# Optimization experiments

Hardware: AMD Instinct MI355X
Metric: run time of the kernel (lower is better)

Reference implementation:

```python
import jax, jax.numpy as jnp
import numpy as np

N = 50000
E = 1600000
IN_DIM = 64
EMB_DIM = 64
DENSE = 128
HEADS = 2
GATD = 64
SLOPE = 0.2


def gat_conv(x, src, dst, W, al, ar, b):
    # DGL GATConv: x [N, Fin], W [Fin, H*D], al/ar/b [H, D]
    n = x.shape[0]
    H, D = al.shape
    z = (x @ W).reshape(n, H, D)                      # [N,H,D]
    el = jnp.sum(z * al, axis=-1)                     # [N,H]
    er = jnp.sum(z * ar, axis=-1)                     # [N,H]
    e = jax.nn.leaky_relu(el[src] + er[dst], SLOPE)   # [E,H]
    # edge softmax grouped by destination node
    m = jax.ops.segment_max(e, dst, num_segments=n)   # [N,H]
    ex = jnp.exp(e - m[dst])                          # [E,H]
    s = jax.ops.segment_sum(ex, dst, num_segments=n)  # [N,H]
    alpha = ex / s[dst]                               # [E,H]
    out = jax.ops.segment_sum(alpha[:, :, None] * z[src], dst, num_segments=n)
    return out + b                                    # [N,H,D]


def setup_inputs() -> dict:
    key = jax.random.key(0)
    ks = jax.random.split(key, 20)
    g = lambda k, sh: jax.random.normal(k, sh, dtype=jnp.float32) * 0.05
    inp = {
        "feat": jax.random.normal(ks[0], (N, IN_DIM), dtype=jnp.float32),
        "node_ids": jax.random.randint(ks[1], (N,), 0, N, dtype=jnp.int32),
        "src": jax.random.randint(ks[2], (E,), 0, N, dtype=jnp.int32),
        "dst": jax.random.randint(ks[3], (E,), 0, N, dtype=jnp.int32),
        "emb": g(ks[4], (N, EMB_DIM)),
        "dense_w": g(ks[5], (IN_DIM + EMB_DIM, DENSE)),
        "dense_b": jnp.zeros((DENSE,), jnp.float32),
        "g1_w": g(ks[6], (DENSE, HEADS * GATD)),
        "g1_al": g(ks[7], (HEADS, GATD)),
        "g1_ar": g(ks[8], (HEADS, GATD)),
        "g1_b": jnp.zeros((HEADS, GATD), jnp.float32),
        "g2_w": g(ks[9], (HEADS * GATD, HEADS * GATD)),
        "g2_al": g(ks[10], (HEADS, GATD)),
        "g2_ar": g(ks[11], (HEADS, GATD)),
        "g2_b": jnp.zeros((HEADS, GATD), jnp.float32),
        "out_w": g(ks[12], (HEADS * GATD, 1)),
        "out_al": g(ks[13], (1, 1)),
        "out_ar": g(ks[14], (1, 1)),
        "out_b": jnp.zeros((1, 1), jnp.float32),
    }
    return inp


def reference(feat, node_ids, src, dst, emb, dense_w, dense_b,
              g1_w, g1_al, g1_ar, g1_b, g2_w, g2_al, g2_ar, g2_b,
              out_w, out_al, out_ar, out_b):
    # embedding concat + initial dense + ReLU
    h = jnp.concatenate([emb[node_ids], feat], axis=-1)   # [N, 128]
    h = jax.nn.relu(h @ dense_w + dense_b)                # [N, 128]
    # GAT layer 1: ReLU then concat heads (reshape N, H*D)
    h = jax.nn.relu(gat_conv(h, src, dst, g1_w, g1_al, g1_ar, g1_b))
    h = h.reshape(h.shape[0], -1)                         # [N, H*D]
    # GAT layer 2
    h = jax.nn.relu(gat_conv(h, src, dst, g2_w, g2_al, g2_ar, g2_b))
    h = h.reshape(h.shape[0], -1)
    # output GAT layer, 1 head, squeeze head dim
    h = gat_conv(h, src, dst, out_w, out_al, out_ar, out_b)  # [N,1,1]
    return h[:, 0, :]                                        # [N,1]
```

## Files before the change

kernel.cpp:

```cpp
#include <hip/hip_runtime.h>
#include <cfloat>
#include <cmath>


#define CBG 256
#define CAPC 12288
#define TILE 2048
#define BIMG 10240

typedef __attribute__((ext_vector_type(8))) short short8v;
typedef __attribute__((ext_vector_type(4))) float f32x4;

__device__ __forceinline__ float lrelu(float x) { return x > 0.f ? x : 0.2f * x; }

__device__ __forceinline__ uint32_t bf16_rne(float f) {
  uint32_t u = __float_as_uint(f);
  return (u + 0x7fffu + ((u >> 16) & 1u)) >> 16;
}
__device__ __forceinline__ uint32_t pack_hilo(float v) {
  uint32_t h = bf16_rne(v);
  float r = v - __uint_as_float(h << 16);
  return (h << 16) | bf16_rne(r);
}

__global__ __launch_bounds__(256) void prep_kernel(
    const float* __restrict__ W0, const float* __restrict__ W1,
    const float* __restrict__ W2, short* __restrict__ Whi0,
    short* __restrict__ Wlo0, short* __restrict__ Whi1, short* __restrict__ Wlo1,
    short* __restrict__ Whi2, short* __restrict__ Wlo2,
    int* __restrict__ scount, int ncb) {
  if (blockIdx.x >= 24) {
    for (int i = threadIdx.x; i < ncb; i += 256) scount[i] = 0;
    return;
  }
  int which = blockIdx.x >> 3;
  const float* W = which == 0 ? W0 : (which == 1 ? W1 : W2);
  short* Whi = which == 0 ? Whi0 : (which == 1 ? Whi1 : Whi2);
  short* Wlo = which == 0 ? Wlo0 : (which == 1 ? Wlo1 : Wlo2);
  int fid = (blockIdx.x & 7) * 256 + threadIdx.x;
  int lane = fid & 63;
  int cq = fid >> 6;
  int q = cq >> 3, c = cq & 7;
  int col = c * 16 + (lane & 15);
  int k0 = q * 32 + (lane >> 4) * 8;
#pragma unroll
  for (int j = 0; j < 8; j++) {
    float v = W[(k0 + j) * 128 + col];
    uint32_t h = bf16_rne(v);
    float r = v - __uint_as_float(h << 16);
    Whi[fid * 8 + j] = (short)h;
    Wlo[fid * 8 + j] = (short)bf16_rne(r);
  }
}

__global__ __launch_bounds__(256) void bucketA_kernel(
    const int* __restrict__ src, const int* __restrict__ dst,
    int* __restrict__ scount, uint32_t* __restrict__ tmp, int e, int ncb) {
  __shared__ int cnt[256];
  __shared__ int lscan[256];
  __shared__ int gbase[256];
  __shared__ uint32_t image[TILE];
  const int t = threadIdx.x;
  const int e0 = blockIdx.x * TILE;
  const int ne = min(TILE, e - e0);

  for (int i = t; i < 256; i += 256) cnt[i] = 0;
  __syncthreads();
  for (int i = t; i < ne; i += 256) atomicAdd(&cnt[dst[e0 + i] >> 8], 1);
  __syncthreads();
  if (t < 64) {
    int carry = 0;
    for (int base = 0; base < ncb; base += 64) {
      int idx = base + t;
      int c = (idx < ncb) ? cnt[idx] : 0;
      int v = c;
#pragma unroll
      for (int off = 1; off < 64; off <<= 1) {
        int u = __shfl_up(v, off, 64);
        if (t >= off) v += u;
      }
      if (idx < ncb) lscan[idx] = carry + v - c;
      carry += __shfl(v, 63, 64);
    }
  }
  __syncthreads();
  for (int b = t; b < ncb; b += 256)
    gbase[b] = (cnt[b] > 0) ? atomicAdd(&scount[b], cnt[b]) : 0;
  __syncthreads();
  for (int b = t; b < ncb; b += 256) cnt[b] = 0;
  __syncthreads();
  for (int i = t; i < ne; i += 256) {
    int d = dst[e0 + i], s = src[e0 + i];
    int b = d >> 8;
    int r = atomicAdd(&cnt[b], 1);
    image[lscan[b] + r] =
        (uint32_t)s | ((uint32_t)(d & 255) << 16) | ((uint32_t)b << 24);
  }
  __syncthreads();
  for (int j = t; j < ne; j += 256) {
    uint32_t w = image[j];
    int b = w >> 24;
    int pos = gbase[b] + (j - lscan[b]);
    if (pos < CAPC) tmp[(size_t)b * CAPC + pos] = w & 0xFFFFFFu;
  }
}

__device__ __forceinline__ void bucketB_body(
    int b, char* smem, const uint32_t* __restrict__ tmp,
    const int* __restrict__ scount, int* __restrict__ row_start,
    int* __restrict__ csr_src, int n, int ncb, int e) {
  int* cnt = (int*)smem;
  int* cur = cnt + 256;
  int* wsum = cur + 256;
  int* s_base = wsum + 4;
  uint32_t* image = (uint32_t*)(smem + 2080);
  const int t = threadIdx.x, lane = t & 63, wid = t >> 6;

  if (t < 64) {
    int part = 0;
    for (int idx = lane; idx < b; idx += 64) part += scount[idx];
#pragma unroll
    for (int off = 32; off; off >>= 1) part += __shfl_xor(part, off, 64);
    if (lane == 0) *s_base = part;
  }
  cnt[t] = 0;
  __syncthreads();
  const int total = min(scount[b], CAPC);
  const int base = *s_base;
  const uint32_t* strm = tmp + (size_t)b * CAPC;

  for (int i = t; i < total; i += 256) atomicAdd(&cnt[(strm[i] >> 16) & 255], 1);
  __syncthreads();
  int c = cnt[t], v = c;
#pragma unroll
  for (int off = 1; off < 64; off <<= 1) {
    int u = __shfl_up(v, off, 64);
    if (lane >= off) v += u;
  }
  if (lane == 63) wsum[wid] = v;
  __syncthreads();
  if (t == 0) {
    int acc = 0;
#pragma unroll
    for (int w = 0; w < 4; w++) { int x = wsum[w]; wsum[w] = acc; acc += x; }
  }
  __syncthreads();
  int ex = wsum[wid] + v - c;
  cur[t] = ex;
  int d = b * CBG + t;
  if (d < n) row_start[d] = base + ex;
  if (b == 0 && t == 0) row_start[n] = e;
  __syncthreads();
  for (int i = t; i < total; i += 256) {
    uint32_t w = strm[i];
    int dl = (w >> 16) & 255;
    int pos = atomicAdd(&cur[dl], 1);
    if (pos < BIMG) image[pos] = w & 0xFFFFu;
    else csr_src[base + pos] = (int)(w & 0xFFFFu);
  }
  __syncthreads();
  const int lim = total < BIMG ? total : BIMG;
  for (int j = t; j < lim; j += 256) csr_src[base + j] = (int)image[j];
}

template <int MODE>
__device__ __forceinline__ void mfmm_body(
    int bid, char* smem,
    const uint32_t* __restrict__ Xp, const short* __restrict__ Whi,
    const short* __restrict__ Wlo, const float* __restrict__ bias,
    uint32_t* __restrict__ Hp, uint32_t* __restrict__ zp,
    float2* __restrict__ el2, float2* __restrict__ er2,
    const float* __restrict__ al, const float* __restrict__ ar, int n,
    const float* __restrict__ emb, const int* __restrict__ ids,
    const float* __restrict__ feat) {
  short* Ahi = (short*)smem;
  short* Alo = Ahi + 64 * 136;
  const int t = threadIdx.x;
  const int nb = bid * 64;

  for (int idx = t; idx < 64 * 32; idx += 256) {
    int nl = idx >> 5, k4 = (idx & 31) << 2;
    int node = nb + nl;
    uint32_t h01 = 0, h23 = 0, l01 = 0, l23 = 0;
    if (node < n) {
      if (MODE == 1) {
        uint4 w = *(const uint4*)&Xp[(size_t)node * 128 + k4];
        h01 = (w.x >> 16) | (w.y & 0xffff0000u);
        l01 = (w.x & 0xffffu) | (w.y << 16);
        h23 = (w.z >> 16) | (w.w & 0xffff0000u);
        l23 = (w.z & 0xffffu) | (w.w << 16);
      } else {
        float4 v;
        if (k4 < 64) v = *(const float4*)&emb[(size_t)ids[node] * 64 + k4];
        else         v = *(const float4*)&feat[(size_t)node * 64 + (k4 - 64)];
        uint32_t a0 = bf16_rne(v.x), a1 = bf16_rne(v.y);
        uint32_t a2 = bf16_rne(v.z), a3 = bf16_rne(v.w);
        h01 = a0 | (a1 << 16);
        h23 = a2 | (a3 << 16);
        l01 = bf16_rne(v.x - __uint_as_float(a0 << 16)) |
              (bf16_rne(v.y - __uint_as_float(a1 << 16)) << 16);
        l23 = bf16_rne(v.z - __uint_as_float(a2 << 16)) |
              (bf16_rne(v.w - __uint_as_float(a3 << 16)) << 16);
      }
    }
    *(uint2*)&Ahi[nl * 136 + k4] = make_uint2(h01, h23);
    *(uint2*)&Alo[nl * 136 + k4] = make_uint2(l01, l23);
  }
  __syncthreads();

  const int lane = t & 63, wv = t >> 6;
  const int r16 = lane & 15, g = lane >> 4;
  const int arow = (wv * 16 + r16) * 136;

  f32x4 acc[8];
#pragma unroll
  for (int c = 0; c < 8; c++) acc[c] = (f32x4){0.f, 0.f, 0.f, 0.f};

#pragma unroll
  for (int q = 0; q < 4; q++) {
    int ka = q * 32 + g * 8;
    short8v ahi = *(const short8v*)&Ahi[arow + ka];
    short8v alo = *(const short8v*)&Alo[arow + ka];
#pragma unroll
    for (int c = 0; c < 8; c++) {
      short8v bhi = *(const short8v*)&Whi[(((q * 8 + c) * 64) + lane) * 8];
      short8v blo = *(const short8v*)&Wlo[(((q * 8 + c) * 64) + lane) * 8];
      acc[c] = __builtin_amdgcn_mfma_f32_16x16x32_bf16(ahi, bhi, acc[c], 0, 0, 0);
      acc[c] = __builtin_amdgcn_mfma_f32_16x16x32_bf16(ahi, blo, acc[c], 0, 0, 0);
      acc[c] = __builtin_amdgcn_mfma_f32_16x16x32_bf16(alo, bhi, acc[c], 0, 0, 0);
    }
  }

  const int node_base = nb + wv * 16;
  if (MODE == 0) {
#pragma unroll
    for (int c = 0; c < 8; c++) {
      int col = c * 16 + r16;
      float bv = bias[col];
#pragma unroll
      for (int r = 0; r < 4; r++) {
        int node = node_base + g * 4 + r;
        if (node < n) {
          float v = fmaxf(acc[c][r] + bv, 0.f);
          Hp[(size_t)node * 128 + col] = pack_hilo(v);
        }
      }
    }
  } else {
    float p0l[4] = {0, 0, 0, 0}, p1l[4] = {0, 0, 0, 0};
    float p0r[4] = {0, 0, 0, 0}, p1r[4] = {0, 0, 0, 0};
#pragma unroll
    for (int c = 0; c < 8; c++) {
      int col = c * 16 + r16;
      float av = al[col], rv = ar[col];
#pragma unroll
      for (int r = 0; r < 4; r++) {
        if (c < 4) { p0l[r] = fmaf(acc[c][r], av, p0l[r]); p0r[r] = fmaf(acc[c][r], rv, p0r[r]); }
        else       { p1l[r] = fmaf(acc[c][r], av, p1l[r]); p1r[r] = fmaf(acc[c][r], rv, p1r[r]); }
      }
    }
#pragma unroll
    for (int c = 0; c < 8; c++) {
#pragma unroll
      for (int r = 0; r < 4; r++) {
        float other = __shfl_xor(acc[c][r], 1, 64);
        int node = node_base + g * 4 + r;
        if (!(lane & 1) && node < n) {
          uint32_t w = bf16_rne(acc[c][r]) | (bf16_rne(other) << 16);
          zp[(size_t)node * 64 + c * 8 + (r16 >> 1)] = w;
        }
      }
    }
#pragma unroll
    for (int off = 1; off < 16; off <<= 1) {
#pragma unroll
      for (int r = 0; r < 4; r++) {
        p0l[r] += __shfl_xor(p0l[r], off, 64);
        p1l[r] += __shfl_xor(p1l[r], off, 64);
        p0r[r] += __shfl_xor(p0r[r], off, 64);
        p1r[r] += __shfl_xor(p1r[r], off, 64);
      }
    }
    if (r16 == 0) {
#pragma unroll
      for (int r = 0; r < 4; r++) {
        int node = node_base + g * 4 + r;
        if (node < n) {
          el2[node] = make_float2(p0l[r], p1l[r]);
          er2[node] = make_float2(p0r[r], p1r[r]);
        }
      }
    }
  }
}

__global__ __launch_bounds__(256) void mfmm0_bktB_kernel(
    const uint32_t* __restrict__ tmp, const int* __restrict__ scount,
    int* __restrict__ row_start, int* __restrict__ csr_src, int ncbB,
    const short* __restrict__ Whi, const short* __restrict__ Wlo,
    const float* __restrict__ bias, uint32_t* __restrict__ Hp, int n, int ncb,
    int e, const float* __restrict__ emb, const int* __restrict__ ids,
    const float* __restrict__ feat) {
  __shared__ __align__(16) char smem[43040];
  if ((int)blockIdx.x < ncbB) {
    bucketB_body(blockIdx.x, smem, tmp, scount, row_start, csr_src, n, ncb, e);
  } else {
    mfmm_body<0>(blockIdx.x - ncbB, smem, nullptr, Whi, Wlo, bias, Hp,
                 nullptr, nullptr, nullptr, nullptr, nullptr, n, emb, ids, feat);
  }
}

__global__ __launch_bounds__(256) void mfmm1_kernel(
    const uint32_t* __restrict__ Xp, const short* __restrict__ Whi,
    const short* __restrict__ Wlo, uint32_t* __restrict__ zp,
    float2* __restrict__ el2, float2* __restrict__ er2,
    const float* __restrict__ al, const float* __restrict__ ar, int n) {
  __shared__ __align__(16) char smem[64 * 136 * 2 * 2];
  mfmm_body<1>(blockIdx.x, smem, Xp, Whi, Wlo, nullptr, nullptr, zp, el2, er2,
               al, ar, n, nullptr, nullptr, nullptr);
}

__global__ void hist_kernel(const int* __restrict__ dst, int* __restrict__ cnt, int e) {
  for (int i = blockIdx.x * blockDim.x + threadIdx.x; i < e; i += gridDim.x * blockDim.x)
    atomicAdd(&cnt[dst[i]], 1);
}
__global__ void scatter_kernel(const int* __restrict__ src, const int* __restrict__ dst,
                               const int* __restrict__ row_start, int* __restrict__ cursor,
                               int* __restrict__ csr_src, int e) {
  for (int i = blockIdx.x * blockDim.x + threadIdx.x; i < e; i += gridDim.x * blockDim.x) {
    int d = dst[i];
    int pos = atomicAdd(&cursor[d], 1);
    csr_src[row_start[d] + pos] = src[i];
  }
}
__global__ __launch_bounds__(1024) void scan1_kernel(const int* __restrict__ cnt,
                                                     int* __restrict__ row_start,
                                                     int* __restrict__ bsum, int n) {
  __shared__ int wsum[16];
  const int t = threadIdx.x, lane = t & 63, wid = t >> 6;
  int i = blockIdx.x * 1024 + t;
  int c = (i < n) ? cnt[i] : 0;
  int v = c;
#pragma unroll
  for (int off = 1; off < 64; off <<= 1) {
    int u = __shfl_up(v, off, 64);
    if (lane >= off) v += u;
  }
  if (lane == 63) wsum[wid] = v;
  __syncthreads();
  if (t == 0) {
    int acc = 0;
#pragma unroll
    for (int w = 0; w < 16; w++) { int x = wsum[w]; wsum[w] = acc; acc += x; }
    bsum[blockIdx.x] = acc;
  }
  __syncthreads();
  if (i < n) row_start[i] = wsum[wid] + v - c;
}
__global__ __launch_bounds__(64) void scan2_kernel(int* __restrict__ bsum, int nb) {
  const int lane = threadIdx.x;
  int carry = 0;
  for (int base = 0; base < nb; base += 64) {
    int idx = base + lane;
    int c = (idx < nb) ? bsum[idx] : 0;
    int v = c;
#pragma unroll
    for (int off = 1; off < 64; off <<= 1) {
      int u = __shfl_up(v, off, 64);
      if (lane >= off) v += u;
    }
    if (idx < nb) bsum[idx] = carry + v - c;
    carry += __shfl(v, 63, 64);
  }
}
__global__ void scan3_kernel(int* __restrict__ row_start, const int* __restrict__ bsum,
                             int n, int e) {
  int i = blockIdx.x * blockDim.x + threadIdx.x;
  if (i < n) row_start[i] += bsum[i >> 10];
  if (i == 0) row_start[n] = e;
}

#define CAP 256
__global__ __launch_bounds__(256) void agg12_kernel(
    const uint32_t* __restrict__ zp, const float2* __restrict__ el2,
    const float2* __restrict__ er2, const int* __restrict__ row_start,
    const int* __restrict__ csr_src, const float* __restrict__ bias,
    uint32_t* __restrict__ Hp,
    const float* __restrict__ ow, const float* __restrict__ oal,
    const float* __restrict__ oar, float* __restrict__ z3,
    float* __restrict__ el3, float* __restrict__ er3, int n, int fuse_out) {
  __shared__ float2 ec[4][CAP];
  __shared__ int sc[4][CAP];
  const int w = threadIdx.x >> 6, lane = threadIdx.x & 63;
  const int node = blockIdx.x * 4 + w;
  const bool valid = node < n;
  int rs = 0, deg = 0;
  float er0 = 0.f, er1 = 0.f;
  if (valid) {
    rs = row_start[node];
    deg = row_start[node + 1] - rs;
    float2 e2 = er2[node];
    er0 = e2.x; er1 = e2.y;
  }
  const int cdeg = deg < CAP ? deg : CAP;

  float sp0 = 0.f, sp1 = 0.f;
  for (int i = lane; i < deg; i += 64) {
    int s = csr_src[rs + i];
    float2 l = el2[s];
    float x0 = __expf(lrelu(l.x + er0));
    float x1 = __expf(lrelu(l.y + er1));
    if (i < CAP) { sc[w][i] = s; ec[w][i] = make_float2(x0, x1); }
    sp0 += x0; sp1 += x1;
  }
#pragma unroll
  for (int off = 32; off; off >>= 1) {
    sp0 += __shfl_xor(sp0, off, 64);
    sp1 += __shfl_xor(sp1, off, 64);
  }
  __syncthreads();

  float ae = 0.f, ao = 0.f;
  int i = 0;
  for (; i + 8 <= cdeg; i += 8) {
    uint32_t zw[8];
    float xh[8];
#pragma unroll
    for (int u = 0; u < 8; u++) {
      int s = sc[w][i + u];
      float2 ex = ec[w][i + u];
      xh[u] = (lane < 32) ? ex.x : ex.y;
      zw[u] = zp[(size_t)s * 64 + lane];
    }
#pragma unroll
    for (int u = 0; u < 8; u++) {
      ae = fmaf(xh[u], __uint_as_float(zw[u] << 16), ae);
      ao = fmaf(xh[u], __uint_as_float(zw[u] & 0xffff0000u), ao);
    }
  }
  for (; i < cdeg; i++) {
    int s = sc[w][i];
    float2 ex = ec[w][i];
    float x = (lane < 32) ? ex.x : ex.y;
    uint32_t zw = zp[(size_t)s * 64 + lane];
    ae = fmaf(x, __uint_as_float(zw << 16), ae);
    ao = fmaf(x, __uint_as_float(zw & 0xffff0000u), ao);
  }
  for (; i < deg; i++) {
    int s = csr_src[rs + i];
    float2 l = el2[s];
    float x0 = __expf(lrelu(l.x + er0));
    float x1 = __expf(lrelu(l.y + er1));
    float x = (lane < 32) ? x0 : x1;
    uint32_t zw = zp[(size_t)s * 64 + lane];
    ae = fmaf(x, __uint_as_float(zw << 16), ae);
    ao = fmaf(x, __uint_as_float(zw & 0xffff0000u), ao);
  }

  if (valid) {
    float sp = (lane < 32) ? sp0 : sp1;
    float2 b2 = reinterpret_cast<const float2*>(bias)[lane];
    float oe, oo;
    if (deg == 0) { oe = b2.x; oo = b2.y; }
    else { oe = ae / sp + b2.x; oo = ao / sp + b2.y; }
    oe = fmaxf(oe, 0.f);
    oo = fmaxf(oo, 0.f);
    if (!fuse_out) {
      *(uint2*)&Hp[(size_t)node * 128 + 2 * lane] =
          make_uint2(pack_hilo(oe), pack_hilo(oo));
    } else {
      float2 w2 = reinterpret_cast<const float2*>(ow)[lane];
      float d = oe * w2.x + oo * w2.y;
#pragma unroll
      for (int off = 32; off; off >>= 1) d += __shfl_xor(d, off, 64);
      if (lane == 0) {
        z3[node] = d;
        el3[node] = d * oal[0];
        er3[node] = d * oar[0];
      }
    }
  }
}

__global__ __launch_bounds__(256) void agg3_kernel(
    const float* __restrict__ z3, const float* __restrict__ el3,
    const float* __restrict__ er3, const int* __restrict__ row_start,
    const int* __restrict__ csr_src, const float* __restrict__ b,
    float* __restrict__ out, int n) {
  int node = blockIdx.x * 8 + (threadIdx.x >> 5);
  int l32 = threadIdx.x & 31;
  if (node >= n) return;
  int rs = row_start[node];
  int deg = row_start[node + 1] - rs;
  float er = er3[node];
  float sp = 0.f, ap = 0.f;
  for (int i = l32; i < deg; i += 32) {
    int s = csr_src[rs + i];
    float ex = __expf(lrelu(el3[s] + er));
    sp += ex;
    ap = fmaf(ex, z3[s], ap);
  }
#pragma unroll
  for (int off = 16; off; off >>= 1) {
    sp += __shfl_xor(sp, off, 64);
    ap += __shfl_xor(ap, off, 64);
  }
  if (l32 == 0) out[node] = (deg == 0) ? b[0] : (ap / sp + b[0]);
}

extern "C" void kernel_launch(void* const* d_in, const int* in_sizes, int n_in,
                              void* d_out, int out_size, void* d_ws, size_t ws_size,
                              hipStream_t stream) {
  const float* feat     = (const float*)d_in[0];
  const int*   node_ids = (const int*)d_in[1];
  const int*   src      = (const int*)d_in[2];
  const int*   dst      = (const int*)d_in[3];
  const float* emb      = (const float*)d_in[4];
  const float* dense_w  = (const float*)d_in[5];
  const float* dense_b  = (const float*)d_in[6];
  const float* g1_w     = (const float*)d_in[7];
  const float* g1_al    = (const float*)d_in[8];
  const float* g1_ar    = (const float*)d_in[9];
  const float* g1_b     = (const float*)d_in[10];
  const float* g2_w     = (const float*)d_in[11];
  const float* g2_al    = (const float*)d_in[12];
  const float* g2_ar    = (const float*)d_in[13];
  const float* g2_b     = (const float*)d_in[14];
  const float* out_w    = (const float*)d_in[15];
  const float* out_al   = (const float*)d_in[16];
  const float* out_ar   = (const float*)d_in[17];
  const float* out_b    = (const float*)d_in[18];
  const int n = in_sizes[0] / 64;
  const int e = in_sizes[2];

  const int ncb = (n + CBG - 1) / CBG;

  char* ws = (char*)d_ws;
  size_t off = 0;
  auto alloc = [&](size_t bytes) -> void* {
    void* p = ws + off;
    off += (bytes + 255) & ~(size_t)255;
    return p;
  };
  uint32_t* Hp       = (uint32_t*)alloc((size_t)n * 128 * 4);
  size_t zp_bytes    = (size_t)n * 64 * 4;
  size_t tmp_bytes   = (size_t)ncb * CAPC * 4;
  uint32_t* zp       = (uint32_t*)alloc(zp_bytes > tmp_bytes ? zp_bytes : tmp_bytes);
  uint32_t* tmp      = zp;
  float2*   el2      = (float2*)alloc((size_t)n * 8);
  float2*   er2      = (float2*)alloc((size_t)n * 8);
  float*    z3       = (float*)alloc((size_t)n * 4);
  float*    el3      = (float*)alloc((size_t)n * 4);
  float*    er3      = (float*)alloc((size_t)n * 4);
  int*      scount   = (int*)alloc((size_t)ncb * 4);
  int*      row_start= (int*)alloc((size_t)(n + 1) * 4);
  int*      csr_src  = (int*)alloc((size_t)e * 4);
  short*    Wd_hi    = (short*)alloc(2048 * 8 * 2);
  short*    Wd_lo    = (short*)alloc(2048 * 8 * 2);
  short*    W1_hi    = (short*)alloc(2048 * 8 * 2);
  short*    W1_lo    = (short*)alloc(2048 * 8 * 2);
  short*    W2_hi    = (short*)alloc(2048 * 8 * 2);
  short*    W2_lo    = (short*)alloc(2048 * 8 * 2);
  int*      cnt      = (int*)alloc((size_t)n * 4);
  int*      cursor   = (int*)alloc((size_t)n * 4);
  const int nblk     = (n + 1023) / 1024;
  int*      bsum     = (int*)alloc((size_t)nblk * 4);

  const int mmgrid = (n + 63) / 64;
  const int ngrid4 = (n + 3) / 4;
  const int ngrid8 = (n + 7) / 8;

  prep_kernel<<<25, 256, 0, stream>>>(dense_w, g1_w, g2_w,
                                      Wd_hi, Wd_lo, W1_hi, W1_lo, W2_hi, W2_lo,
                                      scount, ncb);

  if (n < 65536) {
    const int natile = (e + TILE - 1) / TILE;
    bucketA_kernel<<<natile, 256, 0, stream>>>(src, dst, scount, tmp, e, ncb);
    mfmm0_bktB_kernel<<<ncb + mmgrid, 256, 0, stream>>>(
        tmp, scount, row_start, csr_src, ncb,
        Wd_hi, Wd_lo, dense_b, Hp, n, ncb, e, emb, node_ids, feat);
  } else {
    hipMemsetAsync(cnt, 0, (size_t)n * 4, stream);
    hipMemsetAsync(cursor, 0, (size_t)n * 4, stream);
    hist_kernel<<<2048, 256, 0, stream>>>(dst, cnt, e);
    scan1_kernel<<<nblk, 1024, 0, stream>>>(cnt, row_start, bsum, n);
    scan2_kernel<<<1, 64, 0, stream>>>(bsum, nblk);
    scan3_kernel<<<(n + 255) / 256, 256, 0, stream>>>(row_start, bsum, n, e);
    scatter_kernel<<<2048, 256, 0, stream>>>(src, dst, row_start, cursor, csr_src, e);
    mfmm0_bktB_kernel<<<mmgrid, 256, 0, stream>>>(
        tmp, scount, row_start, csr_src, 0,
        Wd_hi, Wd_lo, dense_b, Hp, n, ncb, e, emb, node_ids, feat);
  }

  mfmm1_kernel<<<mmgrid, 256, 0, stream>>>(Hp, W1_hi, W1_lo, zp, el2, er2,
                                           g1_al, g1_ar, n);
  agg12_kernel<<<ngrid4, 256, 0, stream>>>(zp, el2, er2, row_start, csr_src, g1_b, Hp,
                                           nullptr, nullptr, nullptr, nullptr, nullptr,
                                           nullptr, n, 0);
  mfmm1_kernel<<<mmgrid, 256, 0, stream>>>(Hp, W2_hi, W2_lo, zp, el2, er2,
                                           g2_al, g2_ar, n);
  agg12_kernel<<<ngrid4, 256, 0, stream>>>(zp, el2, er2, row_start, csr_src, g2_b, nullptr,
                                           out_w, out_al, out_ar, z3, el3, er3, n, 1);
  agg3_kernel<<<ngrid8, 256, 0, stream>>>(z3, el3, er3, row_start, csr_src, out_b,
                                          (float*)d_out, n);
}
```

Measured before the change: 237.8 us.

## Sort CSR neighbors coarsely by source range and double bucketing tile

The per-bucket CSR build now counts keys made of destination row plus the top three bits of the source id. Each row's neighbor list therefore comes out grouped into eight source-id ranges, which should give the later gather of source features better cache locality. The first bucketing pass also processes twice as many edges per block. In exchange, the scan and counter arrays grow eightfold in shared memory, the bucket kernel's LDS footprint rises and may lower occupancy, and the first pass runs fewer, larger blocks.

```diff
diff --git a/kernel.cpp b/kernel.cpp
--- a/kernel.cpp
+++ b/kernel.cpp
@@ -5,7 +5,7 @@
 
 #define CBG 256
 #define CAPC 12288
-#define TILE 2048
+#define TILE 4096
 #define BIMG 10240
 
 typedef __attribute__((ext_vector_type(8))) short short8v;
@@ -108,12 +108,11 @@
 __device__ __forceinline__ void bucketB_body(
     int b, char* smem, const uint32_t* __restrict__ tmp,
     const int* __restrict__ scount, int* __restrict__ row_start,
-    int* __restrict__ csr_src, int n, int ncb, int e) {
-  int* cnt = (int*)smem;
-  int* cur = cnt + 256;
-  int* wsum = cur + 256;
+    int* __restrict__ csr_src, int n, int ncb, int e, int sshift) {
+  int* cnt2 = (int*)smem;
+  int* wsum = cnt2 + 2048;
   int* s_base = wsum + 4;
-  uint32_t* image = (uint32_t*)(smem + 2080);
+  uint32_t* image = (uint32_t*)(smem + 8224);
   const int t = threadIdx.x, lane = t & 63, wid = t >> 6;
 
   if (t < 64) {
@@ -123,15 +122,24 @@
     for (int off = 32; off; off >>= 1) part += __shfl_xor(part, off, 64);
     if (lane == 0) *s_base = part;
   }
-  cnt[t] = 0;
+#pragma unroll
+  for (int j = 0; j < 8; j++) cnt2[t * 8 + j] = 0;
   __syncthreads();
   const int total = min(scount[b], CAPC);
   const int base = *s_base;
   const uint32_t* strm = tmp + (size_t)b * CAPC;
 
-  for (int i = t; i < total; i += 256) atomicAdd(&cnt[(strm[i] >> 16) & 255], 1);
-  __syncthreads();
-  int c = cnt[t], v = c;
+  for (int i = t; i < total; i += 256) {
+    uint32_t w = strm[i];
+    int key = (((w >> 16) & 255) << 3) + ((w & 0xFFFFu) >> sshift);
+    atomicAdd(&cnt2[key], 1);
+  }
+  __syncthreads();
+  int c8[8];
+  int run = 0;
+#pragma unroll
+  for (int j = 0; j < 8; j++) { int x = cnt2[t * 8 + j]; c8[j] = run; run += x; }
+  int c = run, v = c;
 #pragma unroll
   for (int off = 1; off < 64; off <<= 1) {
     int u = __shfl_up(v, off, 64);
@@ -146,17 +154,19 @@
   }
   __syncthreads();
   int ex = wsum[wid] + v - c;
-  cur[t] = ex;
+#pragma unroll
+  for (int j = 0; j < 8; j++) cnt2[t * 8 + j] = ex + c8[j];
   int d = b * CBG + t;
   if (d < n) row_start[d] = base + ex;
   if (b == 0 && t == 0) row_start[n] = e;
   __syncthreads();
   for (int i = t; i < total; i += 256) {
     uint32_t w = strm[i];
-    int dl = (w >> 16) & 255;
-    int pos = atomicAdd(&cur[dl], 1);
-    if (pos < BIMG) image[pos] = w & 0xFFFFu;
-    else csr_src[base + pos] = (int)(w & 0xFFFFu);
+    uint32_t s = w & 0xFFFFu;
+    int key = (((w >> 16) & 255) << 3) + (s >> sshift);
+    int pos = atomicAdd(&cnt2[key], 1);
+    if (pos < BIMG) image[pos] = s;
+    else csr_src[base + pos] = (int)s;
   }
   __syncthreads();
   const int lim = total < BIMG ? total : BIMG;
@@ -299,11 +309,12 @@
     int* __restrict__ row_start, int* __restrict__ csr_src, int ncbB,
     const short* __restrict__ Whi, const short* __restrict__ Wlo,
     const float* __restrict__ bias, uint32_t* __restrict__ Hp, int n, int ncb,
-    int e, const float* __restrict__ emb, const int* __restrict__ ids,
+    int e, int sshift, const float* __restrict__ emb, const int* __restrict__ ids,
     const float* __restrict__ feat) {
-  __shared__ __align__(16) char smem[43040];
+  __shared__ __align__(16) char smem[49200];
   if ((int)blockIdx.x < ncbB) {
-    bucketB_body(blockIdx.x, smem, tmp, scount, row_start, csr_src, n, ncb, e);
+    bucketB_body(blockIdx.x, smem, tmp, scount, row_start, csr_src, n, ncb, e,
+                 sshift);
   } else {
     mfmm_body<0>(blockIdx.x - ncbB, smem, nullptr, Whi, Wlo, bias, Hp,
                  nullptr, nullptr, nullptr, nullptr, nullptr, n, emb, ids, feat);
@@ -534,6 +545,9 @@
   const int e = in_sizes[2];
 
   const int ncb = (n + CBG - 1) / CBG;
+  int lg = 0;
+  while ((1 << lg) < n) lg++;
+  const int sshift = lg > 3 ? lg - 3 : 0;
 
   char* ws = (char*)d_ws;
   size_t off = 0;
@@ -579,7 +593,7 @@
     bucketA_kernel<<<natile, 256, 0, stream>>>(src, dst, scount, tmp, e, ncb);
     mfmm0_bktB_kernel<<<ncb + mmgrid, 256, 0, stream>>>(
         tmp, scount, row_start, csr_src, ncb,
-        Wd_hi, Wd_lo, dense_b, Hp, n, ncb, e, emb, node_ids, feat);
+        Wd_hi, Wd_lo, dense_b, Hp, n, ncb, e, sshift, emb, node_ids, feat);
   } else {
     hipMemsetAsync(cnt, 0, (size_t)n * 4, stream);
     hipMemsetAsync(cursor, 0, (size_t)n * 4, stream);
@@ -590,7 +604,7 @@
     scatter_kernel<<<2048, 256, 0, stream>>>(src, dst, row_start, cursor, csr_src, e);
     mfmm0_bktB_kernel<<<mmgrid, 256, 0, stream>>>(
         tmp, scount, row_start, csr_src, 0,
-        Wd_hi, Wd_lo, dense_b, Hp, n, ncb, e, emb, node_ids, feat);
+        Wd_hi, Wd_lo, dense_b, Hp, n, ncb, e, sshift, emb, node_ids, feat);
   }
 
   mfmm1_kernel<<<mmgrid, 256, 0, stream>>>(Hp, W1_hi, W1_lo, zp, el2, er2,
```

Measured after the change: 232.9 us. 2.1% less time.
